# Optimization experiments

Hardware: AMD Instinct MI355X
Metric: run time of the kernel (lower is better)

Reference implementation:

```python
import jax, jax.numpy as jnp
import numpy as np

L = 2
NB = (L + 1) ** 2      # 9 spherical-harmonic basis components
C = 256                # in_channels == out_channels
MID = C // 4           # 64, mid_channels in the FF
N = 4096               # nodes
K = 16                 # neighbors (neighbor_cg)


def _real_sh_l2(rel):
    # Real spherical harmonics up to l=2 of normalized edge directions. rel: [N,K,3] -> [N,K,9]
    r = jnp.sqrt(jnp.sum(rel * rel, axis=-1, keepdims=True))
    d = rel / (r + 1e-8)
    x, y, z = d[..., 0], d[..., 1], d[..., 2]
    c0 = 0.28209479177387814
    c1 = 0.4886025119029199
    c2 = 1.0925484305920792
    c2b = 0.31539156525252005
    c2c = 0.5462742152960396
    return jnp.stack([
        jnp.full_like(x, c0),
        c1 * y, c1 * z, c1 * x,
        c2 * x * y, c2 * y * z, c2b * (3.0 * z * z - 1.0), c2 * x * z, c2c * (x * x - y * y),
    ], axis=-1)


def setup_inputs() -> dict:
    key = jax.random.key(0)
    ks = jax.random.split(key, 8)
    return {
        "s_feats": jax.random.normal(ks[0], (N, NB, C), jnp.float32),
        "s_points": jax.random.normal(ks[1], (N, 3), jnp.float32),
        "cg": jax.random.normal(ks[2], (NB, NB, NB), jnp.float32) * 0.1,  # CG coefficient buffer
        "W_proj": jax.random.normal(ks[3], (C, C), jnp.float32) / np.sqrt(C),
        "ln_w": jnp.ones((L + 1, C), jnp.float32),
        "ln_b": jnp.zeros((C,), jnp.float32),
        "W_ff1": jax.random.normal(ks[4], (C, MID), jnp.float32) / np.sqrt(C),
        "W_gate": jax.random.normal(ks[5], (MID, MID * (L + 1)), jnp.float32) / np.sqrt(MID),
        "W_ff2": jax.random.normal(ks[6], (MID, C), jnp.float32) / np.sqrt(MID),
        "neighbor_indices": jax.random.randint(ks[7], (N, K), 0, N),
    }


def _forward(s_feats, s_points, cg, W_proj, ln_w, ln_b, W_ff1, W_gate, W_ff2, neighbor_indices):
    # --- CGConv: project, gather neighbors, SH of edge directions, CG tensor product, mean-aggregate ---
    h = jnp.einsum('nic,co->nio', s_feats, W_proj)               # [N,9,C]
    nbr = h[neighbor_indices]                                    # [N,K,9,C] irregular gather
    rel = s_points[neighbor_indices] - s_points[:, None, :]      # [N,K,3]
    sh = _real_sh_l2(rel)                                        # [N,K,9]
    x = jnp.einsum('nkic,nkj,ijo->noc', nbr, sh, cg) / K         # [N,9,C]
    # --- residual add of input (linear3 == Identity since in_channels == out_channels) ---
    x = x + s_feats
    shortcut = x
    # --- EquivariantLayerNormV2: per-degree RMS norm; mean-center + bias only on l=0 ---
    outs = []
    for l in range(L + 1):
        f = x[:, l * l:(l + 1) * (l + 1), :]                     # [N,2l+1,C]
        if l == 0:
            f = f - jnp.mean(f, axis=-1, keepdims=True)
        nrm = jnp.mean(f * f, axis=(1, 2), keepdims=True)
        f = f * jax.lax.rsqrt(nrm + 1e-5) * ln_w[l][None, None, :]
        if l == 0:
            f = f + ln_b[None, None, :]
        outs.append(f)
    y = jnp.concatenate(outs, axis=1)
    # --- FF: Linear -> Gate_3j -> Linear, residual ---
    z = jnp.einsum('nic,cm->nim', y, W_ff1)                      # [N,9,MID]
    after = z[:, 0, :] @ W_gate                                  # [N, MID*(L+1)]
    t0 = jax.nn.silu(after[:, :MID])
    mult = jax.nn.sigmoid(after[:, MID:])                        # [N, MID*L]
    gated = [t0[:, None, :]]
    for l in range(1, L + 1):
        gated.append(z[:, l * l:(l + 1) * (l + 1), :] * mult[:, None, (l - 1) * MID:l * MID])
    z = jnp.concatenate(gated, axis=1)                           # [N,9,MID]
    return jnp.einsum('nim,mc->nic', z, W_ff2) + shortcut


def reference(s_feats, s_points, cg, W_proj, ln_w, ln_b, W_ff1, W_gate, W_ff2, neighbor_indices):
    return _forward(s_feats, s_points, cg, W_proj, ln_w, ln_b, W_ff1, W_gate, W_ff2, neighbor_indices)
```

## Files before the change

kernel.cpp:

```cpp
#include <hip/hip_runtime.h>
#include <hip/hip_bf16.h>

#define N_PTS  4096
#define NB     9
#define C      256
#define MID    64
#define KNBR   16
#define NROWS  (N_PTS * NB)

typedef __attribute__((ext_vector_type(8))) short          short8;
typedef __attribute__((ext_vector_type(4))) float          f32x4;
typedef __attribute__((ext_vector_type(4))) unsigned short ush4;
typedef __attribute__((ext_vector_type(8))) unsigned short ush8;

static __device__ __forceinline__ unsigned short f2bf(float f) {
    union { __hip_bfloat16 h; unsigned short u; } cv;
    cv.h = __float2bfloat16(f);
    return cv.u;
}
static __device__ __forceinline__ float bf2f(unsigned short s) {
    union { unsigned u; float f; } v; v.u = ((unsigned)s) << 16;
    return v.f;
}
static __device__ __forceinline__ unsigned packbf(float a, float b) {
    return (unsigned)f2bf(a) | ((unsigned)f2bf(b) << 16);
}

#define LDK 40
__global__ __launch_bounds__(256) void k_proj(const float* __restrict__ A,
                                              const float* __restrict__ W,
                                              unsigned short* __restrict__ H) {
    __shared__ unsigned short As[128 * LDK];
    __shared__ unsigned short Bs[128 * LDK];
    const int tid = threadIdx.x;
    const int r0  = blockIdx.x * 128;
    const int n0  = blockIdx.y * 128;
    const int wave = tid >> 6, lane = tid & 63;
    const int wm = wave >> 1, wn = wave & 1;
    const int lr = lane & 15, lg = lane >> 4;

    f32x4 acc[4][4];
#pragma unroll
    for (int a = 0; a < 4; ++a)
#pragma unroll
        for (int b = 0; b < 4; ++b) acc[a][b] = (f32x4){0.f, 0.f, 0.f, 0.f};

    for (int k0 = 0; k0 < C; k0 += 32) {
        __syncthreads();
#pragma unroll
        for (int rep = 0; rep < 4; ++rep) {
            const int e   = rep * 256 + tid;
            const int row = e >> 3;
            const int c4  = (e & 7) << 2;
            const float4 v = *reinterpret_cast<const float4*>(&A[(size_t)(r0 + row) * C + k0 + c4]);
            ush4 s = { f2bf(v.x), f2bf(v.y), f2bf(v.z), f2bf(v.w) };
            *reinterpret_cast<ush4*>(&As[row * LDK + c4]) = s;
        }
#pragma unroll
        for (int rep = 0; rep < 4; ++rep) {
            const int e = rep * 256 + tid;
            const int k = e >> 5;
            const int j = (e & 31) << 2;
            const float4 v = *reinterpret_cast<const float4*>(&W[(size_t)(k0 + k) * C + n0 + j]);
            Bs[(j + 0) * LDK + k] = f2bf(v.x);
            Bs[(j + 1) * LDK + k] = f2bf(v.y);
            Bs[(j + 2) * LDK + k] = f2bf(v.z);
            Bs[(j + 3) * LDK + k] = f2bf(v.w);
        }
        __syncthreads();

        short8 af[4], bfr[4];
#pragma unroll
        for (int mf = 0; mf < 4; ++mf)
            af[mf] = *reinterpret_cast<const short8*>(&As[(wm * 64 + mf * 16 + lr) * LDK + lg * 8]);
#pragma unroll
        for (int nf = 0; nf < 4; ++nf)
            bfr[nf] = *reinterpret_cast<const short8*>(&Bs[(wn * 64 + nf * 16 + lr) * LDK + lg * 8]);
#pragma unroll
        for (int mf = 0; mf < 4; ++mf)
#pragma unroll
            for (int nf = 0; nf < 4; ++nf)
                acc[mf][nf] = __builtin_amdgcn_mfma_f32_16x16x32_bf16(af[mf], bfr[nf], acc[mf][nf], 0, 0, 0);
    }
#pragma unroll
    for (int mf = 0; mf < 4; ++mf)
#pragma unroll
        for (int nf = 0; nf < 4; ++nf) {
            const int col = n0 + wn * 64 + nf * 16 + lr;
#pragma unroll
            for (int r = 0; r < 4; ++r) {
                const int row = r0 + wm * 64 + mf * 16 + lg * 4 + r;
                H[(size_t)row * C + col] = f2bf(acc[mf][nf][r]);
            }
        }
}

__global__ __launch_bounds__(256) void k_cg_ln(const unsigned short* __restrict__ Hb,
                                               const float* __restrict__ s_feats,
                                               const float* __restrict__ pts,
                                               const float* __restrict__ cg,
                                               const int*   __restrict__ nbr,
                                               const float* __restrict__ ln_w,
                                               const float* __restrict__ ln_b,
                                               unsigned short* __restrict__ Xb,
                                               unsigned short* __restrict__ Yb) {
    __shared__ unsigned short Bs[256 * 40];
    __shared__ unsigned short wT[16 * 168];
    __shared__ float sh_s[KNBR][NB];
    __shared__ int   idx_s[KNBR];
    __shared__ float red_s[2][4];

    float* const cg_s = reinterpret_cast<float*>(Bs);

    const int tid  = threadIdx.x;
    const int n    = blockIdx.x;
    const int wv   = tid >> 6;
    const int lane = tid & 63;
    const int g16  = lane >> 4;
    const int l16  = lane & 15;

    {
        unsigned* w32 = reinterpret_cast<unsigned*>(wT);
        for (int e = tid; e < (16 * 168) / 2; e += 256) w32[e] = 0u;
    }
    for (int e = tid; e < 729; e += 256) cg_s[e] = cg[e];
    if (tid < KNBR) {
        const int idx = nbr[n * KNBR + tid];
        idx_s[tid] = idx;
        const float px = pts[idx * 3 + 0] - pts[n * 3 + 0];
        const float py = pts[idx * 3 + 1] - pts[n * 3 + 1];
        const float pz = pts[idx * 3 + 2] - pts[n * 3 + 2];
        const float r  = sqrtf(px * px + py * py + pz * pz);
        const float iv = 1.f / (r + 1e-8f);
        const float dx = px * iv, dy = py * iv, dz = pz * iv;
        const float c1 = 0.4886025119029199f;
        const float c2 = 1.0925484305920792f;
        sh_s[tid][0] = 0.28209479177387814f;
        sh_s[tid][1] = c1 * dy;
        sh_s[tid][2] = c1 * dz;
        sh_s[tid][3] = c1 * dx;
        sh_s[tid][4] = c2 * dx * dy;
        sh_s[tid][5] = c2 * dy * dz;
        sh_s[tid][6] = 0.31539156525252005f * (3.f * dz * dz - 1.f);
        sh_s[tid][7] = c2 * dx * dz;
        sh_s[tid][8] = 0.5462742152960396f * (dx * dx - dy * dy);
    }
    __syncthreads();

    const int r = tid & 31;
    const int s = tid >> 5;

    ush8 q0, q1, q2, q3;
    {
        const int ki = r;
        const int kk = ki / 9;
        const int ii = ki - kk * 9;
        const unsigned short* hrow = Hb + (size_t)(idx_s[kk] * NB + ii) * C + s * 32;
        q0 = *reinterpret_cast<const ush8*>(hrow + 0);
        q1 = *reinterpret_cast<const ush8*>(hrow + 8);
        q2 = *reinterpret_cast<const ush8*>(hrow + 16);
        q3 = *reinterpret_cast<const ush8*>(hrow + 24);
    }

    for (int t = tid; t < 144 * 9; t += 256) {
        const int ki = t / 9;
        const int o  = t - ki * 9;
        const int kk = ki / 9;
        const int ii = ki - kk * 9;
        float sv = 0.f;
#pragma unroll
        for (int j = 0; j < 9; ++j) sv = fmaf(sh_s[kk][j], cg_s[ii * 81 + j * 9 + o], sv);
        wT[o * 168 + ki] = f2bf(sv);
    }

    f32x4 acc[4];
#pragma unroll
    for (int i = 0; i < 4; ++i) acc[i] = (f32x4){0.f, 0.f, 0.f, 0.f};

    for (int cc = 0; cc < 5; ++cc) {
        const int nrows = (cc == 4) ? 16 : 32;

        __syncthreads();

        if (r < nrows) {
            const unsigned short* qe;
            qe = reinterpret_cast<const unsigned short*>(&q0);
#pragma unroll
            for (int e = 0; e < 8; ++e) Bs[(s * 32 + 0 * 8 + e) * 40 + r] = qe[e];
            qe = reinterpret_cast<const unsigned short*>(&q1);
#pragma unroll
            for (int e = 0; e < 8; ++e) Bs[(s * 32 + 1 * 8 + e) * 40 + r] = qe[e];
            qe = reinterpret_cast<const unsigned short*>(&q2);
#pragma unroll
            for (int e = 0; e < 8; ++e) Bs[(s * 32 + 2 * 8 + e) * 40 + r] = qe[e];
            qe = reinterpret_cast<const unsigned short*>(&q3);
#pragma unroll
            for (int e = 0; e < 8; ++e) Bs[(s * 32 + 3 * 8 + e) * 40 + r] = qe[e];
        }

        if (cc < 4) {
            const int kin   = (cc + 1) * 32 + r;
            const bool vldn = (kin < 144);
            if (vldn) {
                const int kk = kin / 9;
                const int ii = kin - kk * 9;
                const unsigned short* hrow = Hb + (size_t)(idx_s[kk] * NB + ii) * C + s * 32;
                q0 = *reinterpret_cast<const ush8*>(hrow + 0);
                q1 = *reinterpret_cast<const ush8*>(hrow + 8);
                q2 = *reinterpret_cast<const ush8*>(hrow + 16);
                q3 = *reinterpret_cast<const ush8*>(hrow + 24);
            }
        }

        __syncthreads();

        const short8 af = *reinterpret_cast<const short8*>(&wT[l16 * 168 + cc * 32 + g16 * 8]);
        short8 bfr[4];
#pragma unroll
        for (int ti = 0; ti < 4; ++ti)
            bfr[ti] = *reinterpret_cast<const short8*>(&Bs[(wv * 64 + ti * 16 + l16) * 40 + g16 * 8]);
#pragma unroll
        for (int ti = 0; ti < 4; ++ti)
            acc[ti] = __builtin_amdgcn_mfma_f32_16x16x32_bf16(af, bfr[ti], acc[ti], 0, 0, 0);
    }

    __syncthreads();
    float* const Dld = reinterpret_cast<float*>(Bs);
#pragma unroll
    for (int ti = 0; ti < 4; ++ti) {
        const int cgl = (wv * 4 + ti) * 16 + l16;
#pragma unroll
        for (int rr = 0; rr < 4; ++rr) {
            const int o = g16 * 4 + rr;
            if (o < 9) Dld[o * 264 + cgl] = acc[ti][rr] * (1.f / (float)KNBR);
        }
    }
    __syncthreads();

    float2 xv[9];
    float s0 = 0.f, s1 = 0.f, s2 = 0.f, s3 = 0.f;
    if (tid < 128) {
        const int c = tid * 2;
        const float* sf = s_feats + (size_t)n * (NB * C) + c;
#pragma unroll
        for (int i = 0; i < 9; ++i) {
            const float2 d  = *reinterpret_cast<const float2*>(&Dld[i * 264 + c]);
            const float2 sv = *reinterpret_cast<const float2*>(&sf[(size_t)i * C]);
            xv[i].x = d.x + sv.x;
            xv[i].y = d.y + sv.y;
        }
        s0 = xv[0].x + xv[0].y;
        s1 = xv[0].x * xv[0].x + xv[0].y * xv[0].y;
#pragma unroll
        for (int o = 1; o < 4; ++o) s2 += xv[o].x * xv[o].x + xv[o].y * xv[o].y;
#pragma unroll
        for (int o = 4; o < 9; ++o) s3 += xv[o].x * xv[o].x + xv[o].y * xv[o].y;
#pragma unroll
        for (int off = 32; off >= 1; off >>= 1) {
            s0 += __shfl_xor(s0, off);
            s1 += __shfl_xor(s1, off);
            s2 += __shfl_xor(s2, off);
            s3 += __shfl_xor(s3, off);
        }
        if (lane == 0) {
            red_s[wv][0] = s0; red_s[wv][1] = s1;
            red_s[wv][2] = s2; red_s[wv][3] = s3;
        }
    }
    __syncthreads();
    if (tid < 128) {
        s0 = red_s[0][0] + red_s[1][0];
        s1 = red_s[0][1] + red_s[1][1];
        s2 = red_s[0][2] + red_s[1][2];
        s3 = red_s[0][3] + red_s[1][3];

        const float mean0 = s0 * (1.f / 256.f);
        const float nrm0  = s1 * (1.f / 256.f) - mean0 * mean0;
        const float nrm1  = s2 * (1.f / 768.f);
        const float nrm2  = s3 * (1.f / 1280.f);
        const float r0v = rsqrtf(nrm0 + 1e-5f);
        const float r1v = rsqrtf(nrm1 + 1e-5f);
        const float r2v = rsqrtf(nrm2 + 1e-5f);

        const int c = tid * 2;
        const float2 lw0 = *reinterpret_cast<const float2*>(ln_w + c);
        const float2 lw1 = *reinterpret_cast<const float2*>(ln_w + C + c);
        const float2 lw2 = *reinterpret_cast<const float2*>(ln_w + 2 * C + c);
        const float2 lb0 = *reinterpret_cast<const float2*>(ln_b + c);

        unsigned* xo = reinterpret_cast<unsigned*>(Xb + (size_t)n * (NB * C));
        unsigned* yo = reinterpret_cast<unsigned*>(Yb + (size_t)n * (NB * C));
#pragma unroll
        for (int i = 0; i < 9; ++i) xo[i * 128 + tid] = packbf(xv[i].x, xv[i].y);
        yo[tid] = packbf((xv[0].x - mean0) * r0v * lw0.x + lb0.x,
                         (xv[0].y - mean0) * r0v * lw0.y + lb0.y);
#pragma unroll
        for (int i = 1; i < 4; ++i)
            yo[i * 128 + tid] = packbf(xv[i].x * r1v * lw1.x, xv[i].y * r1v * lw1.y);
#pragma unroll
        for (int i = 4; i < 9; ++i)
            yo[i * 128 + tid] = packbf(xv[i].x * r2v * lw2.x, xv[i].y * r2v * lw2.y);
    }
}

__global__ __launch_bounds__(256) void k_ff1(const unsigned short* __restrict__ Yb,
                                             const float* __restrict__ W1,
                                             unsigned short* __restrict__ Zb) {
    __shared__ unsigned short As[128 * LDK];
    __shared__ unsigned short Bs[64 * LDK];
    const int tid = threadIdx.x;
    const int r0  = blockIdx.x * 128;
    const int wave = tid >> 6, lane = tid & 63;
    const int wm = wave >> 1, wn = wave & 1;
    const int lr = lane & 15, lg = lane >> 4;

    f32x4 acc[4][2];
#pragma unroll
    for (int a = 0; a < 4; ++a) { acc[a][0] = (f32x4){0.f,0.f,0.f,0.f}; acc[a][1] = (f32x4){0.f,0.f,0.f,0.f}; }

    for (int k0 = 0; k0 < C; k0 += 32) {
        __syncthreads();
#pragma unroll
        for (int rep = 0; rep < 4; ++rep) {
            const int e   = rep * 256 + tid;
            const int row = e >> 3;
            const int c4  = (e & 7) << 2;
            ush4 s = *reinterpret_cast<const ush4*>(&Yb[(size_t)(r0 + row) * C + k0 + c4]);
            *reinterpret_cast<ush4*>(&As[row * LDK + c4]) = s;
        }
#pragma unroll
        for (int rep = 0; rep < 2; ++rep) {
            const int e = rep * 256 + tid;
            const int k = e >> 4;
            const int j = (e & 15) << 2;
            const float4 v = *reinterpret_cast<const float4*>(&W1[(size_t)(k0 + k) * MID + j]);
            Bs[(j + 0) * LDK + k] = f2bf(v.x);
            Bs[(j + 1) * LDK + k] = f2bf(v.y);
            Bs[(j + 2) * LDK + k] = f2bf(v.z);
            Bs[(j + 3) * LDK + k] = f2bf(v.w);
        }
        __syncthreads();

        short8 af[4], bfr[2];
#pragma unroll
        for (int mf = 0; mf < 4; ++mf)
            af[mf] = *reinterpret_cast<const short8*>(&As[(wm * 64 + mf * 16 + lr) * LDK + lg * 8]);
#pragma unroll
        for (int nf = 0; nf < 2; ++nf)
            bfr[nf] = *reinterpret_cast<const short8*>(&Bs[(wn * 32 + nf * 16 + lr) * LDK + lg * 8]);
#pragma unroll
        for (int mf = 0; mf < 4; ++mf)
#pragma unroll
            for (int nf = 0; nf < 2; ++nf)
                acc[mf][nf] = __builtin_amdgcn_mfma_f32_16x16x32_bf16(af[mf], bfr[nf], acc[mf][nf], 0, 0, 0);
    }
#pragma unroll
    for (int mf = 0; mf < 4; ++mf)
#pragma unroll
        for (int nf = 0; nf < 2; ++nf) {
            const int col = wn * 32 + nf * 16 + lr;
#pragma unroll
            for (int r = 0; r < 4; ++r) {
                const int row = r0 + wm * 64 + mf * 16 + lg * 4 + r;
                Zb[(size_t)row * MID + col] = f2bf(acc[mf][nf][r]);
            }
        }
}

__global__ __launch_bounds__(192) void k_gate(const unsigned short* __restrict__ Zb,
                                              const float* __restrict__ Wg,
                                              float* __restrict__ G) {
    __shared__ float wgs[64 * 192];
    __shared__ float z0s[16 * 64];
    const int tid = threadIdx.x;
    const int n0  = blockIdx.x * 16;

    for (int e = tid; e < 64 * 192; e += 192) wgs[e] = Wg[e];
    for (int e = tid; e < 16 * 64; e += 192) {
        const int r = e >> 6, m = e & 63;
        z0s[e] = bf2f(Zb[(size_t)(n0 + r) * (NB * MID) + m]);
    }
    __syncthreads();

    const int j = tid;
    for (int r = 0; r < 16; ++r) {
        float acc = 0.f;
        for (int m0 = 0; m0 < 64; m0 += 4) {
            const float4 zv = *reinterpret_cast<const float4*>(&z0s[r * 64 + m0]);
            acc = fmaf(zv.x, wgs[(m0 + 0) * 192 + j], acc);
            acc = fmaf(zv.y, wgs[(m0 + 1) * 192 + j], acc);
            acc = fmaf(zv.z, wgs[(m0 + 2) * 192 + j], acc);
            acc = fmaf(zv.w, wgs[(m0 + 3) * 192 + j], acc);
        }
        const float sig = 1.f / (1.f + expf(-acc));
        G[(size_t)(n0 + r) * 192 + j] = (j < 64) ? acc * sig : sig;
    }
}

#define LDK64 72
__global__ __launch_bounds__(256) void k_final(const unsigned short* __restrict__ Zb,
                                               const float* __restrict__ G,
                                               const float* __restrict__ W2,
                                               const unsigned short* __restrict__ Xb,
                                               float* __restrict__ OUT) {
    __shared__ unsigned short As[128 * LDK64];
    __shared__ unsigned short Bs[128 * LDK64];
    const int tid = threadIdx.x;
    const int r0  = blockIdx.x * 128;
    const int n0  = blockIdx.y * 128;
    const int wave = tid >> 6, lane = tid & 63;
    const int wm = wave >> 1, wn = wave & 1;
    const int lr = lane & 15, lg = lane >> 4;

    {
        const int arow = tid >> 1;
        const int kh   = (tid & 1) * 32;
        const int grow = r0 + arow;
        const int nn   = grow / 9;
        const int ii   = grow - nn * 9;
        if (ii == 0) {
            const float* gp = &G[(size_t)nn * 192 + kh];
#pragma unroll
            for (int j = 0; j < 32; j += 4) {
                const float4 g = *reinterpret_cast<const float4*>(&gp[j]);
                ush4 s = { f2bf(g.x), f2bf(g.y), f2bf(g.z), f2bf(g.w) };
                *reinterpret_cast<ush4*>(&As[arow * LDK64 + kh + j]) = s;
            }
        } else {
            const float* gm = &G[(size_t)nn * 192 + ((ii < 4) ? 64 : 128) + kh];
            const unsigned short* zr = &Zb[(size_t)nn * (NB * MID) + ii * MID + kh];
#pragma unroll
            for (int j = 0; j < 32; j += 4) {
                const ush4 zv = *reinterpret_cast<const ush4*>(&zr[j]);
                const float4 g = *reinterpret_cast<const float4*>(&gm[j]);
                ush4 s = { f2bf(bf2f(zv.x) * g.x), f2bf(bf2f(zv.y) * g.y),
                           f2bf(bf2f(zv.z) * g.z), f2bf(bf2f(zv.w) * g.w) };
                *reinterpret_cast<ush4*>(&As[arow * LDK64 + kh + j]) = s;
            }
        }
    }
#pragma unroll
    for (int rep = 0; rep < 8; ++rep) {
        const int e = rep * 256 + tid;
        const int k = e >> 5;
        const int j = (e & 31) << 2;
        const float4 v = *reinterpret_cast<const float4*>(&W2[(size_t)k * C + n0 + j]);
        Bs[(j + 0) * LDK64 + k] = f2bf(v.x);
        Bs[(j + 1) * LDK64 + k] = f2bf(v.y);
        Bs[(j + 2) * LDK64 + k] = f2bf(v.z);
        Bs[(j + 3) * LDK64 + k] = f2bf(v.w);
    }
    __syncthreads();

    f32x4 acc[4][4];
#pragma unroll
    for (int a = 0; a < 4; ++a)
#pragma unroll
        for (int b = 0; b < 4; ++b) acc[a][b] = (f32x4){0.f, 0.f, 0.f, 0.f};

#pragma unroll
    for (int ks = 0; ks < 2; ++ks) {
        short8 af[4], bfr[4];
#pragma unroll
        for (int mf = 0; mf < 4; ++mf)
            af[mf] = *reinterpret_cast<const short8*>(&As[(wm * 64 + mf * 16 + lr) * LDK64 + ks * 32 + lg * 8]);
#pragma unroll
        for (int nf = 0; nf < 4; ++nf)
            bfr[nf] = *reinterpret_cast<const short8*>(&Bs[(wn * 64 + nf * 16 + lr) * LDK64 + ks * 32 + lg * 8]);
#pragma unroll
        for (int mf = 0; mf < 4; ++mf)
#pragma unroll
            for (int nf = 0; nf < 4; ++nf)
                acc[mf][nf] = __builtin_amdgcn_mfma_f32_16x16x32_bf16(af[mf], bfr[nf], acc[mf][nf], 0, 0, 0);
    }

#pragma unroll
    for (int mf = 0; mf < 4; ++mf)
#pragma unroll
        for (int nf = 0; nf < 4; ++nf) {
            const int col = n0 + wn * 64 + nf * 16 + lr;
#pragma unroll
            for (int r = 0; r < 4; ++r) {
                const int row = r0 + wm * 64 + mf * 16 + lg * 4 + r;
                OUT[(size_t)row * C + col] = acc[mf][nf][r] + bf2f(Xb[(size_t)row * C + col]);
            }
        }
}

extern "C" void kernel_launch(void* const* d_in, const int* in_sizes, int n_in,
                              void* d_out, int out_size, void* d_ws, size_t ws_size,
                              hipStream_t stream) {
    const float* s_feats = (const float*)d_in[0];
    const float* s_pts   = (const float*)d_in[1];
    const float* cg      = (const float*)d_in[2];
    const float* W_proj  = (const float*)d_in[3];
    const float* ln_w    = (const float*)d_in[4];
    const float* ln_b    = (const float*)d_in[5];
    const float* W_ff1   = (const float*)d_in[6];
    const float* W_gate  = (const float*)d_in[7];
    const float* W_ff2   = (const float*)d_in[8];
    const int*   nbr     = (const int*)d_in[9];
    float* out = (float*)d_out;

    unsigned short* Hb = (unsigned short*)d_ws;
    unsigned short* Xb = Hb + (size_t)NROWS * C;
    unsigned short* Yb = Xb + (size_t)NROWS * C;
    unsigned short* Zb = Yb + (size_t)NROWS * C;
    float* G = (float*)(Zb + (size_t)NROWS * MID);

    k_proj  <<<dim3(NROWS / 128, 2), 256, 0, stream>>>(s_feats, W_proj, Hb);
    k_cg_ln <<<N_PTS,                256, 0, stream>>>(Hb, s_feats, s_pts, cg, nbr, ln_w, ln_b, Xb, Yb);
    k_ff1   <<<NROWS / 128,          256, 0, stream>>>(Yb, W_ff1, Zb);
    k_gate  <<<N_PTS / 16,           192, 0, stream>>>(Zb, W_gate, G);
    k_final <<<dim3(NROWS / 128, 2), 256, 0, stream>>>(Zb, G, W_ff2, Xb, out);
}
```

Before: 129.4 us.

## Defer layernorm into ff1 load, stash bf16 s_feats, double-buffer neighbor gathers

k_proj now also writes a bf16 copy of s_feats, so k_cg_ln reads the residual in half precision instead of fp32. k_cg_ln no longer writes the normalized Y tensor. It stores only per-node reduction sums, and k_ff1 applies the layernorm while loading X into shared memory. The gather loop is unrolled with two register buffers so that each chunk is loaded two steps ahead. These changes cut global traffic (one full NROWS×C bf16 write and read is removed) in exchange for extra arithmetic in ff1, and the bf16 residual adds rounding error.

Result: slower. 153.7 us (+18.8%).

```diff
diff --git a/kernel.cpp b/kernel.cpp
--- a/kernel.cpp
+++ b/kernel.cpp
@@ -10,6 +10,7 @@
 
 typedef __attribute__((ext_vector_type(8))) short          short8;
 typedef __attribute__((ext_vector_type(4))) float          f32x4;
+typedef __attribute__((ext_vector_type(2))) float          f32x2;
 typedef __attribute__((ext_vector_type(4))) unsigned short ush4;
 typedef __attribute__((ext_vector_type(8))) unsigned short ush8;
 
@@ -22,6 +23,12 @@
     union { unsigned u; float f; } v; v.u = ((unsigned)s) << 16;
     return v.f;
 }
+static __device__ __forceinline__ f32x2 bf2x2(unsigned u) {
+    union { unsigned u; float f; } lo, hi;
+    lo.u = u << 16;
+    hi.u = u & 0xffff0000u;
+    return (f32x2){lo.f, hi.f};
+}
 static __device__ __forceinline__ unsigned packbf(float a, float b) {
     return (unsigned)f2bf(a) | ((unsigned)f2bf(b) << 16);
 }
@@ -29,12 +36,14 @@
 #define LDK 40
 __global__ __launch_bounds__(256) void k_proj(const float* __restrict__ A,
                                               const float* __restrict__ W,
-                                              unsigned short* __restrict__ H) {
+                                              unsigned short* __restrict__ H,
+                                              unsigned short* __restrict__ SFB) {
     __shared__ unsigned short As[128 * LDK];
     __shared__ unsigned short Bs[128 * LDK];
     const int tid = threadIdx.x;
     const int r0  = blockIdx.x * 128;
     const int n0  = blockIdx.y * 128;
+    const bool emit_sfb = (blockIdx.y == 0);
     const int wave = tid >> 6, lane = tid & 63;
     const int wm = wave >> 1, wn = wave & 1;
     const int lr = lane & 15, lg = lane >> 4;
@@ -55,6 +64,8 @@
             const float4 v = *reinterpret_cast<const float4*>(&A[(size_t)(r0 + row) * C + k0 + c4]);
             ush4 s = { f2bf(v.x), f2bf(v.y), f2bf(v.z), f2bf(v.w) };
             *reinterpret_cast<ush4*>(&As[row * LDK + c4]) = s;
+            if (emit_sfb)
+                *reinterpret_cast<ush4*>(&SFB[(size_t)(r0 + row) * C + k0 + c4]) = s;
         }
 #pragma unroll
         for (int rep = 0; rep < 4; ++rep) {
@@ -95,15 +106,43 @@
         }
 }
 
+static __device__ __forceinline__ void load_chunk(const unsigned short* __restrict__ Hb,
+                                                  const int* idx_s, int ki, int s,
+                                                  ush8& q0, ush8& q1, ush8& q2, ush8& q3) {
+    const int kk = ki / 9;
+    const int ii = ki - kk * 9;
+    const unsigned short* hrow = Hb + (size_t)(idx_s[kk] * NB + ii) * C + s * 32;
+    q0 = *reinterpret_cast<const ush8*>(hrow + 0);
+    q1 = *reinterpret_cast<const ush8*>(hrow + 8);
+    q2 = *reinterpret_cast<const ush8*>(hrow + 16);
+    q3 = *reinterpret_cast<const ush8*>(hrow + 24);
+}
+static __device__ __forceinline__ void stage_chunk(unsigned short* Bs, int r, int s, int nrows,
+                                                   ush8 q0, ush8 q1, ush8 q2, ush8 q3) {
+    if (r < nrows) {
+        const unsigned short* qe;
+        qe = reinterpret_cast<const unsigned short*>(&q0);
+#pragma unroll
+        for (int e = 0; e < 8; ++e) Bs[(s * 32 + e) * 40 + r] = qe[e];
+        qe = reinterpret_cast<const unsigned short*>(&q1);
+#pragma unroll
+        for (int e = 0; e < 8; ++e) Bs[(s * 32 + 8 + e) * 40 + r] = qe[e];
+        qe = reinterpret_cast<const unsigned short*>(&q2);
+#pragma unroll
+        for (int e = 0; e < 8; ++e) Bs[(s * 32 + 16 + e) * 40 + r] = qe[e];
+        qe = reinterpret_cast<const unsigned short*>(&q3);
+#pragma unroll
+        for (int e = 0; e < 8; ++e) Bs[(s * 32 + 24 + e) * 40 + r] = qe[e];
+    }
+}
+
 __global__ __launch_bounds__(256) void k_cg_ln(const unsigned short* __restrict__ Hb,
-                                               const float* __restrict__ s_feats,
+                                               const unsigned short* __restrict__ SFB,
                                                const float* __restrict__ pts,
                                                const float* __restrict__ cg,
                                                const int*   __restrict__ nbr,
-                                               const float* __restrict__ ln_w,
-                                               const float* __restrict__ ln_b,
                                                unsigned short* __restrict__ Xb,
-                                               unsigned short* __restrict__ Yb) {
+                                               float* __restrict__ scr) {
     __shared__ unsigned short Bs[256 * 40];
     __shared__ unsigned short wT[16 * 168];
     __shared__ float sh_s[KNBR][NB];
@@ -150,17 +189,9 @@
     const int r = tid & 31;
     const int s = tid >> 5;
 
-    ush8 q0, q1, q2, q3;
-    {
-        const int ki = r;
-        const int kk = ki / 9;
-        const int ii = ki - kk * 9;
-        const unsigned short* hrow = Hb + (size_t)(idx_s[kk] * NB + ii) * C + s * 32;
-        q0 = *reinterpret_cast<const ush8*>(hrow + 0);
-        q1 = *reinterpret_cast<const ush8*>(hrow + 8);
-        q2 = *reinterpret_cast<const ush8*>(hrow + 16);
-        q3 = *reinterpret_cast<const ush8*>(hrow + 24);
-    }
+    ush8 qa0, qa1, qa2, qa3, qb0, qb1, qb2, qb3;
+    load_chunk(Hb, idx_s, 0 * 32 + r, s, qa0, qa1, qa2, qa3);
+    load_chunk(Hb, idx_s, 1 * 32 + r, s, qb0, qb1, qb2, qb3);
 
     for (int t = tid; t < 144 * 9; t += 256) {
         const int ki = t / 9;
@@ -177,52 +208,42 @@
 #pragma unroll
     for (int i = 0; i < 4; ++i) acc[i] = (f32x4){0.f, 0.f, 0.f, 0.f};
 
-    for (int cc = 0; cc < 5; ++cc) {
-        const int nrows = (cc == 4) ? 16 : 32;
-
-        __syncthreads();
-
-        if (r < nrows) {
-            const unsigned short* qe;
-            qe = reinterpret_cast<const unsigned short*>(&q0);
-#pragma unroll
-            for (int e = 0; e < 8; ++e) Bs[(s * 32 + 0 * 8 + e) * 40 + r] = qe[e];
-            qe = reinterpret_cast<const unsigned short*>(&q1);
-#pragma unroll
-            for (int e = 0; e < 8; ++e) Bs[(s * 32 + 1 * 8 + e) * 40 + r] = qe[e];
-            qe = reinterpret_cast<const unsigned short*>(&q2);
-#pragma unroll
-            for (int e = 0; e < 8; ++e) Bs[(s * 32 + 2 * 8 + e) * 40 + r] = qe[e];
-            qe = reinterpret_cast<const unsigned short*>(&q3);
-#pragma unroll
-            for (int e = 0; e < 8; ++e) Bs[(s * 32 + 3 * 8 + e) * 40 + r] = qe[e];
-        }
-
-        if (cc < 4) {
-            const int kin   = (cc + 1) * 32 + r;
-            const bool vldn = (kin < 144);
-            if (vldn) {
-                const int kk = kin / 9;
-                const int ii = kin - kk * 9;
-                const unsigned short* hrow = Hb + (size_t)(idx_s[kk] * NB + ii) * C + s * 32;
-                q0 = *reinterpret_cast<const ush8*>(hrow + 0);
-                q1 = *reinterpret_cast<const ush8*>(hrow + 8);
-                q2 = *reinterpret_cast<const ush8*>(hrow + 16);
-                q3 = *reinterpret_cast<const ush8*>(hrow + 24);
-            }
-        }
-
-        __syncthreads();
-
-        const short8 af = *reinterpret_cast<const short8*>(&wT[l16 * 168 + cc * 32 + g16 * 8]);
-        short8 bfr[4];
-#pragma unroll
-        for (int ti = 0; ti < 4; ++ti)
-            bfr[ti] = *reinterpret_cast<const short8*>(&Bs[(wv * 64 + ti * 16 + l16) * 40 + g16 * 8]);
-#pragma unroll
-        for (int ti = 0; ti < 4; ++ti)
-            acc[ti] = __builtin_amdgcn_mfma_f32_16x16x32_bf16(af, bfr[ti], acc[ti], 0, 0, 0);
-    }
+#define MFMA_STEP(cc)                                                                   \
+    do {                                                                                \
+        const short8 af = *reinterpret_cast<const short8*>(&wT[l16 * 168 + (cc) * 32 + g16 * 8]); \
+        short8 bfr[4];                                                                  \
+        _Pragma("unroll")                                                               \
+        for (int ti = 0; ti < 4; ++ti)                                                  \
+            bfr[ti] = *reinterpret_cast<const short8*>(&Bs[(wv * 64 + ti * 16 + l16) * 40 + g16 * 8]); \
+        _Pragma("unroll")                                                               \
+        for (int ti = 0; ti < 4; ++ti)                                                  \
+            acc[ti] = __builtin_amdgcn_mfma_f32_16x16x32_bf16(af, bfr[ti], acc[ti], 0, 0, 0); \
+    } while (0)
+
+    __syncthreads();
+    stage_chunk(Bs, r, s, 32, qa0, qa1, qa2, qa3);
+    load_chunk(Hb, idx_s, 2 * 32 + r, s, qa0, qa1, qa2, qa3);
+    __syncthreads();
+    MFMA_STEP(0);
+    __syncthreads();
+    stage_chunk(Bs, r, s, 32, qb0, qb1, qb2, qb3);
+    load_chunk(Hb, idx_s, 3 * 32 + r, s, qb0, qb1, qb2, qb3);
+    __syncthreads();
+    MFMA_STEP(1);
+    __syncthreads();
+    stage_chunk(Bs, r, s, 32, qa0, qa1, qa2, qa3);
+    if (r < 16) load_chunk(Hb, idx_s, 4 * 32 + r, s, qa0, qa1, qa2, qa3);
+    __syncthreads();
+    MFMA_STEP(2);
+    __syncthreads();
+    stage_chunk(Bs, r, s, 32, qb0, qb1, qb2, qb3);
+    __syncthreads();
+    MFMA_STEP(3);
+    __syncthreads();
+    stage_chunk(Bs, r, s, 16, qa0, qa1, qa2, qa3);
+    __syncthreads();
+    MFMA_STEP(4);
+#undef MFMA_STEP
 
     __syncthreads();
     float* const Dld = reinterpret_cast<float*>(Bs);
@@ -237,20 +258,23 @@
     }
     __syncthreads();
 
-    float2 xv[9];
-    float s0 = 0.f, s1 = 0.f, s2 = 0.f, s3 = 0.f;
     if (tid < 128) {
         const int c = tid * 2;
-        const float* sf = s_feats + (size_t)n * (NB * C) + c;
+        const unsigned* sfr = reinterpret_cast<const unsigned*>(SFB + (size_t)n * (NB * C));
+        float2 xv[9];
 #pragma unroll
         for (int i = 0; i < 9; ++i) {
-            const float2 d  = *reinterpret_cast<const float2*>(&Dld[i * 264 + c]);
-            const float2 sv = *reinterpret_cast<const float2*>(&sf[(size_t)i * C]);
-            xv[i].x = d.x + sv.x;
-            xv[i].y = d.y + sv.y;
-        }
-        s0 = xv[0].x + xv[0].y;
-        s1 = xv[0].x * xv[0].x + xv[0].y * xv[0].y;
+            const f32x2 sv = bf2x2(sfr[i * 128 + tid]);
+            xv[i].x = Dld[i * 264 + c]     + sv.x;
+            xv[i].y = Dld[i * 264 + c + 1] + sv.y;
+        }
+        unsigned* xo = reinterpret_cast<unsigned*>(Xb + (size_t)n * (NB * C));
+#pragma unroll
+        for (int i = 0; i < 9; ++i) xo[i * 128 + tid] = packbf(xv[i].x, xv[i].y);
+
+        float s0 = xv[0].x + xv[0].y;
+        float s1 = xv[0].x * xv[0].x + xv[0].y * xv[0].y;
+        float s2 = 0.f, s3 = 0.f;
 #pragma unroll
         for (int o = 1; o < 4; ++o) s2 += xv[o].x * xv[o].x + xv[o].y * xv[o].y;
 #pragma unroll
@@ -268,42 +292,19 @@
         }
     }
     __syncthreads();
-    if (tid < 128) {
-        s0 = red_s[0][0] + red_s[1][0];
-        s1 = red_s[0][1] + red_s[1][1];
-        s2 = red_s[0][2] + red_s[1][2];
-        s3 = red_s[0][3] + red_s[1][3];
-
-        const float mean0 = s0 * (1.f / 256.f);
-        const float nrm0  = s1 * (1.f / 256.f) - mean0 * mean0;
-        const float nrm1  = s2 * (1.f / 768.f);
-        const float nrm2  = s3 * (1.f / 1280.f);
-        const float r0v = rsqrtf(nrm0 + 1e-5f);
-        const float r1v = rsqrtf(nrm1 + 1e-5f);
-        const float r2v = rsqrtf(nrm2 + 1e-5f);
-
-        const int c = tid * 2;
-        const float2 lw0 = *reinterpret_cast<const float2*>(ln_w + c);
-        const float2 lw1 = *reinterpret_cast<const float2*>(ln_w + C + c);
-        const float2 lw2 = *reinterpret_cast<const float2*>(ln_w + 2 * C + c);
-        const float2 lb0 = *reinterpret_cast<const float2*>(ln_b + c);
-
-        unsigned* xo = reinterpret_cast<unsigned*>(Xb + (size_t)n * (NB * C));
-        unsigned* yo = reinterpret_cast<unsigned*>(Yb + (size_t)n * (NB * C));
-#pragma unroll
-        for (int i = 0; i < 9; ++i) xo[i * 128 + tid] = packbf(xv[i].x, xv[i].y);
-        yo[tid] = packbf((xv[0].x - mean0) * r0v * lw0.x + lb0.x,
-                         (xv[0].y - mean0) * r0v * lw0.y + lb0.y);
-#pragma unroll
-        for (int i = 1; i < 4; ++i)
-            yo[i * 128 + tid] = packbf(xv[i].x * r1v * lw1.x, xv[i].y * r1v * lw1.y);
-#pragma unroll
-        for (int i = 4; i < 9; ++i)
-            yo[i * 128 + tid] = packbf(xv[i].x * r2v * lw2.x, xv[i].y * r2v * lw2.y);
-    }
-}
-
-__global__ __launch_bounds__(256) void k_ff1(const unsigned short* __restrict__ Yb,
+    if (tid == 0) {
+        float* sp = scr + (size_t)n * 4;
+        sp[0] = red_s[0][0] + red_s[1][0];
+        sp[1] = red_s[0][1] + red_s[1][1];
+        sp[2] = red_s[0][2] + red_s[1][2];
+        sp[3] = red_s[0][3] + red_s[1][3];
+    }
+}
+
+__global__ __launch_bounds__(256) void k_ff1(const unsigned short* __restrict__ Xb,
+                                             const float* __restrict__ scr,
+                                             const float* __restrict__ ln_w,
+                                             const float* __restrict__ ln_b,
                                              const float* __restrict__ W1,
                                              unsigned short* __restrict__ Zb) {
     __shared__ unsigned short As[128 * LDK];
@@ -314,6 +315,27 @@
     const int wm = wave >> 1, wn = wave & 1;
     const int lr = lane & 15, lg = lane >> 4;
 
+    float mu_[4], rv_[4];
+    int   cls_[4];
+#pragma unroll
+    for (int rep = 0; rep < 4; ++rep) {
+        const int row = r0 + ((rep * 256 + tid) >> 3);
+        const int nn  = row / 9;
+        const int ii  = row - nn * 9;
+        const float* sp = scr + (size_t)nn * 4;
+        const float a0 = sp[0], a1 = sp[1], a2 = sp[2], a3 = sp[3];
+        if (ii == 0) {
+            const float mu = a0 * (1.f / 256.f);
+            mu_[rep] = mu;
+            rv_[rep] = rsqrtf(a1 * (1.f / 256.f) - mu * mu + 1e-5f);
+            cls_[rep] = 0;
+        } else if (ii < 4) {
+            mu_[rep] = 0.f; rv_[rep] = rsqrtf(a2 * (1.f / 768.f) + 1e-5f); cls_[rep] = 1;
+        } else {
+            mu_[rep] = 0.f; rv_[rep] = rsqrtf(a3 * (1.f / 1280.f) + 1e-5f); cls_[rep] = 2;
+        }
+    }
+
     f32x4 acc[4][2];
 #pragma unroll
     for (int a = 0; a < 4; ++a) { acc[a][0] = (f32x4){0.f,0.f,0.f,0.f}; acc[a][1] = (f32x4){0.f,0.f,0.f,0.f}; }
@@ -325,7 +347,18 @@
             const int e   = rep * 256 + tid;
             const int row = e >> 3;
             const int c4  = (e & 7) << 2;
-            ush4 s = *reinterpret_cast<const ush4*>(&Yb[(size_t)(r0 + row) * C + k0 + c4]);
+            const ush4 xq = *reinterpret_cast<const ush4*>(&Xb[(size_t)(r0 + row) * C + k0 + c4]);
+            const float4 lw = *reinterpret_cast<const float4*>(&ln_w[cls_[rep] * C + k0 + c4]);
+            const float mu = mu_[rep], rv = rv_[rep];
+            float yx = (bf2f(xq.x) - mu) * rv * lw.x;
+            float yy = (bf2f(xq.y) - mu) * rv * lw.y;
+            float yz = (bf2f(xq.z) - mu) * rv * lw.z;
+            float yw = (bf2f(xq.w) - mu) * rv * lw.w;
+            if (cls_[rep] == 0) {
+                const float4 lb = *reinterpret_cast<const float4*>(&ln_b[k0 + c4]);
+                yx += lb.x; yy += lb.y; yz += lb.z; yw += lb.w;
+            }
+            ush4 s = { f2bf(yx), f2bf(yy), f2bf(yz), f2bf(yw) };
             *reinterpret_cast<ush4*>(&As[row * LDK + c4]) = s;
         }
 #pragma unroll
@@ -502,15 +535,16 @@
     const int*   nbr     = (const int*)d_in[9];
     float* out = (float*)d_out;
 
-    unsigned short* Hb = (unsigned short*)d_ws;
-    unsigned short* Xb = Hb + (size_t)NROWS * C;
-    unsigned short* Yb = Xb + (size_t)NROWS * C;
-    unsigned short* Zb = Yb + (size_t)NROWS * C;
-    float* G = (float*)(Zb + (size_t)NROWS * MID);
-
-    k_proj  <<<dim3(NROWS / 128, 2), 256, 0, stream>>>(s_feats, W_proj, Hb);
-    k_cg_ln <<<N_PTS,                256, 0, stream>>>(Hb, s_feats, s_pts, cg, nbr, ln_w, ln_b, Xb, Yb);
-    k_ff1   <<<NROWS / 128,          256, 0, stream>>>(Yb, W_ff1, Zb);
+    unsigned short* Hb  = (unsigned short*)d_ws;
+    unsigned short* Xb  = Hb + (size_t)NROWS * C;
+    unsigned short* Zb  = Xb + (size_t)NROWS * C;
+    unsigned short* SFB = Zb + (size_t)NROWS * MID;
+    float* G   = (float*)(SFB + (size_t)NROWS * C);
+    float* scr = G + (size_t)N_PTS * 192;
+
+    k_proj  <<<dim3(NROWS / 128, 2), 256, 0, stream>>>(s_feats, W_proj, Hb, SFB);
+    k_cg_ln <<<N_PTS,                256, 0, stream>>>(Hb, SFB, s_pts, cg, nbr, Xb, scr);
+    k_ff1   <<<NROWS / 128,          256, 0, stream>>>(Xb, scr, ln_w, ln_b, W_ff1, Zb);
     k_gate  <<<N_PTS / 16,           192, 0, stream>>>(Zb, W_gate, G);
     k_final <<<dim3(NROWS / 128, 2), 256, 0, stream>>>(Zb, G, W_ff2, Xb, out);
 }
```
